# Performance work log

Hardware: AMD Instinct MI355X
Metric: run time of the kernel (lower is better)

The kernel has to match this reference:

```python
import jax, jax.numpy as jnp
import numpy as np

P = 4        # number of sequence pairs (half batch)
L = 512      # sequence length
D = 64       # embedding dim
NUM_CLASSES = 4
BIAS_INIT = 10.0


def setup_inputs() -> dict:
    key = jax.random.key(0)
    k1, k2, k3 = jax.random.split(key, 3)
    seqs_logits = jax.random.normal(k1, (2 * P, L, D), dtype=jnp.float32)
    ordinal_weight = jax.random.normal(k2, (1, NUM_CLASSES), dtype=jnp.float32)
    ordinal_bias = jax.random.normal(k3, (NUM_CLASSES,), dtype=jnp.float32) + BIAS_INIT
    return {"seqs_logits": seqs_logits, "ordinal_weight": ordinal_weight,
            "ordinal_bias": ordinal_bias}


def reference(seqs_logits, ordinal_weight, ordinal_bias):
    half = seqs_logits.shape[0] // 2
    z0 = seqs_logits[:half]          # [P, L0, D]
    z1 = seqs_logits[half:2 * half]  # [P, L1, D]

    def score_plus(z0_i, z1_i):
        # pairwise negative L1 distance: [L0, L1]
        s = -jnp.sum(jnp.abs(z0_i[:, None, :] - z1_i[None, :, :]), axis=-1)
        a = jax.nn.softmax(s, axis=1)   # row-wise alignment
        b = jax.nn.softmax(s, axis=0)   # column-wise alignment
        c = a + b - a * b               # symmetric soft alignment
        c_val = jnp.sum(c * s) / jnp.sum(c)
        logit = c_val * ordinal_weight + ordinal_bias  # [1, 4]
        return logit.reshape(-1)        # [4]

    return jax.vmap(score_plus)(z0, z1)  # [P, 4]
```

## Files before the change

### kernel.cpp

```cpp
#include <hip/hip_runtime.h>
#include <math.h>

#define P 4
#define L 512
#define D 64
#define NC 4
#define RS 68
#define SHIFT 64.0f
#define NBLK 512

#define ROWP_O 0
#define COLP_O 32768
#define ACC_O  49152
#define CNT_O  49280
#define SV_O   49664

__global__ __launch_bounds__(256, 2) void dist_stats(const float* __restrict__ z,
                                                     float* __restrict__ ws) {
    const int bx = blockIdx.x;
    const int pair = bx >> 7, jb = (bx >> 4) & 7, kh = bx & 15;
    const int tid = threadIdx.x;
    const int tx = tid & 7;
    const int ty = tid >> 3;
    const int wave = tid >> 6, lane = tid & 63;

    if (bx == 0) {
        if (tid < 4) { ws[ACC_O + tid * 32] = 0.0f; ws[ACC_O + tid * 32 + 1] = 0.0f; }
        else if (tid == 4) ((int*)(ws + CNT_O))[0] = 0;
    }

    __shared__ float jt[64][RS];
    __shared__ float kt[32][RS];
    __shared__ float csred[4][32];

    {
        const float4* z0t = (const float4*)(z + ((size_t)pair * L + jb * 64) * D);
        const float4* z1t = (const float4*)(z + ((size_t)(P + pair) * L + kh * 32) * D);
        #pragma unroll
        for (int i = 0; i < 4; ++i) {
            const int li = i * 256 + tid;
            *(float4*)&jt[li >> 4][(li & 15) * 4] = z0t[li];
        }
        #pragma unroll
        for (int i = 0; i < 2; ++i) {
            const int li = i * 256 + tid;
            *(float4*)&kt[li >> 4][(li & 15) * 4] = z1t[li];
        }
    }
    __syncthreads();

    float acc[2][4];
    #pragma unroll
    for (int r = 0; r < 2; ++r)
        #pragma unroll
        for (int q = 0; q < 4; ++q) acc[r][q] = 0.f;
    #pragma unroll
    for (int c = 0; c < 16; ++c) {
        float4 jv[2], kv[4];
        #pragma unroll
        for (int r = 0; r < 2; ++r) jv[r] = *(const float4*)&jt[ty + 32 * r][c * 4];
        #pragma unroll
        for (int q = 0; q < 4; ++q) kv[q] = *(const float4*)&kt[tx + 8 * q][c * 4];
        #pragma unroll
        for (int r = 0; r < 2; ++r)
            #pragma unroll
            for (int q = 0; q < 4; ++q)
                acc[r][q] += fabsf(jv[r].x - kv[q].x) + fabsf(jv[r].y - kv[q].y)
                           + fabsf(jv[r].z - kv[q].z) + fabsf(jv[r].w - kv[q].w);
    }

    {
        float4* svb = (float4*)(ws + SV_O + (size_t)bx * 2048 + tid * 8);
        #pragma unroll
        for (int r = 0; r < 2; ++r) {
            float4 v;
            v.x = -acc[r][0]; v.y = -acc[r][1]; v.z = -acc[r][2]; v.w = -acc[r][3];
            svb[r] = v;
        }
    }

    float rs_[2] = {0.f, 0.f};
    float cs_[4] = {0.f, 0.f, 0.f, 0.f};
    #pragma unroll
    for (int r = 0; r < 2; ++r)
        #pragma unroll
        for (int q = 0; q < 4; ++q) {
            const float e = __expf(SHIFT - acc[r][q]);
            rs_[r] += e;
            cs_[q] += e;
        }
    #pragma unroll
    for (int off = 1; off <= 4; off <<= 1)
        #pragma unroll
        for (int r = 0; r < 2; ++r) rs_[r] += __shfl_xor(rs_[r], off);
    if (tx == 0) {
        #pragma unroll
        for (int r = 0; r < 2; ++r)
            ws[ROWP_O + (pair * 16 + kh) * 512 + jb * 64 + ty + 32 * r] = rs_[r];
    }
    #pragma unroll
    for (int off = 8; off <= 32; off <<= 1)
        #pragma unroll
        for (int q = 0; q < 4; ++q) cs_[q] += __shfl_xor(cs_[q], off);
    if (lane < 8) {
        #pragma unroll
        for (int q = 0; q < 4; ++q) csred[wave][tx + 8 * q] = cs_[q];
    }
    __syncthreads();
    if (tid < 32)
        ws[COLP_O + (pair * 8 + jb) * 512 + kh * 32 + tid]
            = csred[0][tid] + csred[1][tid] + csred[2][tid] + csred[3][tid];
}

__global__ __launch_bounds__(256) void c_accum_final(float* __restrict__ ws,
                                                     const float* __restrict__ w,
                                                     const float* __restrict__ bias,
                                                     float* __restrict__ out) {
    const int bx = blockIdx.x;
    const int pair = bx >> 7, jb = (bx >> 4) & 7, kh = bx & 15;
    const int tid = threadIdx.x;
    const int tx = tid & 7, ty = tid >> 3;
    const int wave = tid >> 6, lane = tid & 63;

    __shared__ float rrcp_s[64], crcp_s[32];
    __shared__ float bred[4][2];
    __shared__ int   last_flag;
    __shared__ float totals[8];

    if (tid < 64) {
        float s = 0.f;
        #pragma unroll
        for (int h = 0; h < 16; ++h)
            s += ws[ROWP_O + (pair * 16 + h) * 512 + jb * 64 + tid];
        rrcp_s[tid] = 1.0f / s;
    } else if (tid < 96) {
        const int kl = tid - 64;
        float s = 0.f;
        #pragma unroll
        for (int b = 0; b < 8; ++b)
            s += ws[COLP_O + (pair * 8 + b) * 512 + kh * 32 + kl];
        crcp_s[kl] = 1.0f / s;
    }
    __syncthreads();

    const float4* svb = (const float4*)(ws + SV_O + (size_t)bx * 2048 + tid * 8);
    float cs = 0.f, cc = 0.f;
    #pragma unroll
    for (int r = 0; r < 2; ++r) {
        const float rr = rrcp_s[ty + 32 * r];
        const float4 sv4 = svb[r];
        const float svs[4] = {sv4.x, sv4.y, sv4.z, sv4.w};
        #pragma unroll
        for (int q = 0; q < 4; ++q) {
            const float cr = crcp_s[tx + 8 * q];
            const float sv = svs[q];
            const float e  = __expf(SHIFT + sv);
            const float a  = e * rr;
            const float b  = e * cr;
            const float c  = a + b - a * b;
            cs += c * sv;
            cc += c;
        }
    }
    #pragma unroll
    for (int off = 1; off <= 32; off <<= 1) {
        cs += __shfl_xor(cs, off);
        cc += __shfl_xor(cc, off);
    }
    if (lane == 0) { bred[wave][0] = cs; bred[wave][1] = cc; }
    __syncthreads();

    if (tid == 0) {
        const float bcs = bred[0][0] + bred[1][0] + bred[2][0] + bred[3][0];
        const float bcc = bred[0][1] + bred[1][1] + bred[2][1] + bred[3][1];
        atomicAdd(&ws[ACC_O + pair * 32],     bcs);
        atomicAdd(&ws[ACC_O + pair * 32 + 1], bcc);
        __builtin_amdgcn_s_waitcnt(0);
        const int old = atomicAdd((int*)(ws + CNT_O), 1);
        last_flag = (old == NBLK - 1) ? 1 : 0;
    }
    __syncthreads();

    if (last_flag) {
        if (tid < 8)
            totals[tid] = atomicAdd(&ws[ACC_O + (tid >> 1) * 32 + (tid & 1)], 0.0f);
        __syncthreads();
        if (tid < P) {
            const float c_val = totals[tid * 2] / totals[tid * 2 + 1];
            #pragma unroll
            for (int cls = 0; cls < NC; ++cls)
                out[tid * NC + cls] = c_val * w[cls] + bias[cls];
        }
    }
}

extern "C" void kernel_launch(void* const* d_in, const int* in_sizes, int n_in,
                              void* d_out, int out_size, void* d_ws, size_t ws_size,
                              hipStream_t stream) {
    const float* z    = (const float*)d_in[0];
    const float* w    = (const float*)d_in[1];
    const float* bias = (const float*)d_in[2];
    float* out = (float*)d_out;
    float* ws  = (float*)d_ws;

    dist_stats   <<<dim3(NBLK), dim3(256), 0, stream>>>(z, ws);
    c_accum_final<<<dim3(NBLK), dim3(256), 0, stream>>>(ws, w, bias, out);
}
```

Measured before the change: 73.26 us.

## Coarsen second kernel to 64 blocks with per-pair completion counters

The accumulation kernel now runs 64 blocks instead of 512. Each block handles one pair and one column chunk and loops over all 8 row blocks, computing row reciprocals for the full 512 rows once in shared memory instead of redundantly per block. The single global completion counter is replaced with per-pair counters on separate cache lines, so each pair finalises independently. This cuts redundant row-sum reads and atomic contention, but leaves far fewer blocks to cover the GPU, which may underuse the CUs.

```diff
diff --git a/kernel.cpp b/kernel.cpp
--- a/kernel.cpp
+++ b/kernel.cpp
@@ -26,7 +26,7 @@
 
     if (bx == 0) {
         if (tid < 4) { ws[ACC_O + tid * 32] = 0.0f; ws[ACC_O + tid * 32 + 1] = 0.0f; }
-        else if (tid == 4) ((int*)(ws + CNT_O))[0] = 0;
+        else if (tid < 8) ((int*)(ws + CNT_O))[(tid - 4) * 32] = 0;
     }
 
     __shared__ float jt[64][RS];
@@ -117,49 +117,58 @@
                                                      const float* __restrict__ bias,
                                                      float* __restrict__ out) {
     const int bx = blockIdx.x;
-    const int pair = bx >> 7, jb = (bx >> 4) & 7, kh = bx & 15;
+    const int pair = bx >> 4, ch = bx & 15;
     const int tid = threadIdx.x;
-    const int tx = tid & 7, ty = tid >> 3;
     const int wave = tid >> 6, lane = tid & 63;
 
-    __shared__ float rrcp_s[64], crcp_s[32];
+    __shared__ float rrcp_s[512];
+    __shared__ float crcp_s[32];
     __shared__ float bred[4][2];
     __shared__ int   last_flag;
-    __shared__ float totals[8];
-
-    if (tid < 64) {
+    __shared__ float totals[2];
+
+    #pragma unroll
+    for (int i = 0; i < 2; ++i) {
+        const int j = i * 256 + tid;
         float s = 0.f;
         #pragma unroll
         for (int h = 0; h < 16; ++h)
-            s += ws[ROWP_O + (pair * 16 + h) * 512 + jb * 64 + tid];
-        rrcp_s[tid] = 1.0f / s;
-    } else if (tid < 96) {
-        const int kl = tid - 64;
+            s += ws[ROWP_O + (pair * 16 + h) * 512 + j];
+        rrcp_s[j] = 1.0f / s;
+    }
+    if (tid < 32) {
         float s = 0.f;
         #pragma unroll
         for (int b = 0; b < 8; ++b)
-            s += ws[COLP_O + (pair * 8 + b) * 512 + kh * 32 + kl];
-        crcp_s[kl] = 1.0f / s;
-    }
-    __syncthreads();
-
-    const float4* svb = (const float4*)(ws + SV_O + (size_t)bx * 2048 + tid * 8);
+            s += ws[COLP_O + (pair * 8 + b) * 512 + ch * 32 + tid];
+        crcp_s[tid] = 1.0f / s;
+    }
+    __syncthreads();
+
     float cs = 0.f, cc = 0.f;
     #pragma unroll
-    for (int r = 0; r < 2; ++r) {
-        const float rr = rrcp_s[ty + 32 * r];
-        const float4 sv4 = svb[r];
-        const float svs[4] = {sv4.x, sv4.y, sv4.z, sv4.w};
-        #pragma unroll
-        for (int q = 0; q < 4; ++q) {
-            const float cr = crcp_s[tx + 8 * q];
-            const float sv = svs[q];
-            const float e  = __expf(SHIFT + sv);
-            const float a  = e * rr;
-            const float b  = e * cr;
-            const float c  = a + b - a * b;
-            cs += c * sv;
-            cc += c;
+    for (int jb = 0; jb < 8; ++jb) {
+        const float4* svb = (const float4*)(ws + SV_O
+                            + (size_t)((pair << 7) | (jb << 4) | ch) * 2048);
+        #pragma unroll
+        for (int i = 0; i < 2; ++i) {
+            const int o4 = i * 256 + tid;
+            const float4 sv4 = svb[o4];
+            const int j = jb * 64 + (o4 >> 4) + 32 * (o4 & 1);
+            const int kb = (o4 >> 1) & 7;
+            const float rr = rrcp_s[j];
+            const float svs[4] = {sv4.x, sv4.y, sv4.z, sv4.w};
+            #pragma unroll
+            for (int q = 0; q < 4; ++q) {
+                const float cr = crcp_s[kb + 8 * q];
+                const float sv = svs[q];
+                const float e  = __expf(SHIFT + sv);
+                const float a  = e * rr;
+                const float b  = e * cr;
+                const float c  = a + b - a * b;
+                cs += c * sv;
+                cc += c;
+            }
         }
     }
     #pragma unroll
@@ -176,20 +185,20 @@
         atomicAdd(&ws[ACC_O + pair * 32],     bcs);
         atomicAdd(&ws[ACC_O + pair * 32 + 1], bcc);
         __builtin_amdgcn_s_waitcnt(0);
-        const int old = atomicAdd((int*)(ws + CNT_O), 1);
-        last_flag = (old == NBLK - 1) ? 1 : 0;
+        const int old = atomicAdd(&((int*)(ws + CNT_O))[pair * 32], 1);
+        last_flag = (old == 15) ? 1 : 0;
     }
     __syncthreads();
 
     if (last_flag) {
-        if (tid < 8)
-            totals[tid] = atomicAdd(&ws[ACC_O + (tid >> 1) * 32 + (tid & 1)], 0.0f);
+        if (tid < 2)
+            totals[tid] = atomicAdd(&ws[ACC_O + pair * 32 + tid], 0.0f);
         __syncthreads();
-        if (tid < P) {
-            const float c_val = totals[tid * 2] / totals[tid * 2 + 1];
+        if (tid == 0) {
+            const float c_val = totals[0] / totals[1];
             #pragma unroll
             for (int cls = 0; cls < NC; ++cls)
-                out[tid * NC + cls] = c_val * w[cls] + bias[cls];
+                out[pair * NC + cls] = c_val * w[cls] + bias[cls];
         }
     }
 }
@@ -203,6 +212,6 @@
     float* out = (float*)d_out;
     float* ws  = (float*)d_ws;
 
-    dist_stats   <<<dim3(NBLK), dim3(256), 0, stream>>>(z, ws);
-    c_accum_final<<<dim3(NBLK), dim3(256), 0, stream>>>(ws, w, bias, out);
+    dist_stats   <<<dim3(NBLK),  dim3(256), 0, stream>>>(z, ws);
+    c_accum_final<<<dim3(P * 16), dim3(256), 0, stream>>>(ws, w, bias, out);
 }
```

Result: faster. 70.62 us (-3.6%).
